# Kernel optimization log

Hardware: AMD Instinct MI355X
Metric: run time of the kernel (lower is better)

Reference implementation:

```python
import jax, jax.numpy as jnp
import numpy as np

jax.config.update("jax_enable_x64", True)  # loss accumulates int64 squared index diffs (~1e14)

PATCH, STRIDE = 7, 1


def extract_patches(img, p, s):
    # img: [b, c, h, w] -> patches [b, N, c*p*p], N = oh*ow (normalize_patch='none')
    pat = jax.lax.conv_general_dilated_patches(img, (p, p), (s, s), 'VALID')  # [b, c*p*p, oh, ow]
    b, d = pat.shape[0], pat.shape[1]
    return pat.reshape(b, d, -1).transpose(0, 2, 1)


def bisect_left(a, v):
    # Exact replica of np.searchsorted(a, v, side='left') binary search,
    # applied (as in the original code) to an UNSORTED int array `a`.
    # a: [N] int, v: [M] int -> [M] insertion indices in [0, N].
    N = a.shape[0]
    lo = jnp.zeros(v.shape, jnp.int64)
    hi = jnp.full(v.shape, N, jnp.int64)
    n_iter = int(np.ceil(np.log2(N))) + 1
    for _ in range(n_iter):
        mid = (lo + hi) // 2
        am = a[jnp.clip(mid, 0, N - 1)]
        go = lo < hi
        pred = am < v
        lo = jnp.where(go & pred, mid + 1, lo)
        hi = jnp.where(go & (~pred), mid, hi)
    return lo


def nearest_vals(a, v):
    # Vectorized find_nearest(a, v_i) for all v_i. a: [N], v: [M].
    N = a.shape[0]
    idx = bisect_left(a, v)
    a_prev = a[jnp.clip(idx - 1, 0, N - 1)]
    a_at = a[jnp.clip(idx, 0, N - 1)]
    take_prev = (idx > 0) & ((idx == N) | (jnp.abs(v - a_prev) < jnp.abs(v - a_at)))
    return jnp.where(take_prev, a_prev, a_at)


def reference(x, y, rand):
    # rand: [b, d, num_proj]; per-batch projection matrix, normalized by unbiased column std
    rand = rand / jnp.std(rand, axis=1, keepdims=True, ddof=1)
    xp = extract_patches(x, PATCH, STRIDE)  # [b, N, d]
    yp = extract_patches(y, PATCH, STRIDE)  # [b, N, d]
    proj_x = jnp.einsum('bnd,bdp->bnp', xp, rand)
    proj_y = jnp.einsum('bnd,bdp->bnp', yp, rand)
    # Original overwrites projections with argsort indices; only j=0 is used
    # because of the early return inside the projection loop.
    ai = jnp.argsort(proj_x[:, :, 0], axis=1).astype(jnp.int64)  # [b, N]
    at = jnp.argsort(proj_y[:, :, 0], axis=1).astype(jnp.int64)  # [b, N]
    nearest = jax.vmap(nearest_vals)(at, ai)  # [b, N]
    N = ai.shape[1]
    per_image = jnp.sum((ai - nearest) ** 2, axis=1) / N  # int sum -> float
    return jnp.mean(per_image)  # batch_reduction='mean'


def setup_inputs() -> dict:
    key = jax.random.key(0)
    k1, k2, k3 = jax.random.split(key, 3)
    b, c, h, w = 4, 3, 256, 256
    d = c * PATCH * PATCH  # 147
    x = jax.random.normal(k1, (b, c, h, w), dtype=jnp.float32)
    y = jax.random.normal(k2, (b, c, h, w), dtype=jnp.float32)
    rand = jax.random.normal(k3, (b, d, 1), dtype=jnp.float32)
    return {"x": x, "y": y, "rand": rand}
```

## Files before the change

kernel.cpp:

```cpp
#include <hip/hip_runtime.h>
#include <stdint.h>

#define OH 250
#define OW 250
#define NPTS (OH*OW)
#define NSEG 4
#define D 147
#define CH 3
#define IMH 256
#define IMW 256
#define NITER 17
#define NBUCK 8192
#define CAP 128
#define SIG0 12.124355652982141

typedef unsigned long long u64;
typedef unsigned int u32;

#define OFF_SREC  0UL
#define OFF_A     33554432UL
#define OFF_WTS   34554432UL
#define OFF_CURS  34559136UL
#define OFF_BASES 34690208UL
#define OFF_SUMS  34821296UL
#define OFF_TICK  34821328UL
#define OFF_OFLOW 34821336UL
#define WS_NEED   34821340UL

__device__ __forceinline__ u64 packd(double f) {
  u64 u = (u64)__double_as_longlong(f);
  return (u & 0x8000000000000000ULL) ? ~u : (u | 0x8000000000000000ULL);
}

__device__ __forceinline__ int bucket_of(u64 rec) {
  u64 t = rec & ~0x1FFFFULL;
  u64 bits = (t & 0x8000000000000000ULL) ? (t & 0x7FFFFFFFFFFFFFFFULL) : ~t;
  double v = __longlong_as_double((long long)bits);
  double z = (v + 4.0 * SIG0) * ((double)NBUCK / (8.0 * SIG0));
  int b = (z <= 0.0) ? 0 : (int)z;
  if (b > NBUCK - 1) b = NBUCK - 1;
  return b;
}

__global__ __launch_bounds__(256) void setup_kern(const float* __restrict__ rnd,
                                                  double* __restrict__ wts,
                                                  u32* __restrict__ curs,
                                                  u64* __restrict__ sums,
                                                  u32* __restrict__ tick,
                                                  u32* __restrict__ oflow) {
  int t = threadIdx.x;
  if (blockIdx.x < 4) {
    int b = blockIdx.x;
    int lane = t & 63;
    double v0 = (double)rnd[b * D + lane];
    double v1 = (double)rnd[b * D + lane + 64];
    double v2 = (lane + 128 < D) ? (double)rnd[b * D + lane + 128] : 0.0;
    double sm = v0 + v1 + v2;
    #pragma unroll
    for (int o = 32; o > 0; o >>= 1) sm += __shfl_xor(sm, o, 64);
    double mean = sm / (double)D;
    double d0 = v0 - mean, d1 = v1 - mean;
    double d2 = (lane + 128 < D) ? (v2 - mean) : 0.0;
    double ss = d0 * d0 + d1 * d1 + d2 * d2;
    #pragma unroll
    for (int o = 32; o > 0; o >>= 1) ss += __shfl_xor(ss, o, 64);
    double stdv = sqrt(ss / (double)(D - 1));
    if (t < 64) {
      wts[b * D + lane] = v0 / stdv;
      wts[b * D + lane + 64] = v1 / stdv;
      if (lane + 128 < D) wts[b * D + lane + 128] = v2 / stdv;
    }
    if (b == 0 && t < 8) ((u32*)sums)[t] = 0u;
    if (b == 0 && t >= 8 && t < 10) tick[t - 8] = 0u;
    if (b == 0 && t == 10) oflow[0] = 0u;
  } else {
    int g = (blockIdx.x - 4) * 1024 + t * 4;
    if (g < NSEG * NBUCK) {
      curs[g] = 0u; curs[g + 1] = 0u; curs[g + 2] = 0u; curs[g + 3] = 0u;
    }
  }
}

__global__ __launch_bounds__(256) void conv_kern(const float* __restrict__ y,
                                                 const double* __restrict__ wts,
                                                 u64* __restrict__ srec,
                                                 u32* __restrict__ curs,
                                                 u32* __restrict__ oflow) {
  __shared__ float tile[CH][22][22];
  __shared__ double wlds[D];
  int b = blockIdx.z;
  const float* in = y + (size_t)b * CH * IMH * IMW;
  int bi = blockIdx.y * 16, bj = blockIdx.x * 16;
  int tid = threadIdx.y * 16 + threadIdx.x;
  if (tid < D) wlds[tid] = wts[b * D + tid];
  for (int c = 0; c < CH; ++c)
    for (int t = tid; t < 22 * 22; t += 256) {
      int rr = t / 22, cc = t - rr * 22;
      int r = bi + rr, col = bj + cc;
      float v = 0.f;
      if (r < IMH && col < IMW) v = in[((size_t)c * IMH + r) * IMW + col];
      tile[c][rr][cc] = v;
    }
  __syncthreads();
  int i = bi + threadIdx.y, j = bj + threadIdx.x;
  if (i < OH && j < OW) {
    double acc = 0.0;
    #pragma unroll
    for (int c = 0; c < CH; ++c) {
      double ac = 0.0;
      #pragma unroll
      for (int ph = 0; ph < 7; ++ph)
        #pragma unroll
        for (int pw = 0; pw < 7; ++pw)
          ac = fma((double)tile[c][threadIdx.y + ph][threadIdx.x + pw],
                   wlds[c * 49 + ph * 7 + pw], ac);
      acc += ac;
    }
    int n = i * OW + j;
    u64 rec = (packd(acc) & ~0x1FFFFULL) | (u64)(u32)n;
    int bk = b * NBUCK + bucket_of(rec);
    u32 pos = atomicAdd(&curs[bk], 1u);
    if (pos < CAP) srec[(size_t)bk * CAP + pos] = rec;
    else atomicOr(oflow, 1u);
  }
}

__global__ __launch_bounds__(1024) void scan_kern(const u32* __restrict__ curs,
                                                  u32* __restrict__ bases,
                                                  u32* __restrict__ oflow) {
  __shared__ u32 part[1024];
  int seg = blockIdx.x, t = threadIdx.x;
  u32 c[8]; u32 run = 0;
  #pragma unroll
  for (int m = 0; m < 8; ++m) {
    u32 v = curs[seg * NBUCK + 8 * t + m];
    c[m] = v > CAP ? CAP : v;
    run += c[m];
  }
  part[t] = run;
  __syncthreads();
  for (int off = 1; off < 1024; off <<= 1) {
    u32 v = (t >= off) ? part[t - off] : 0u;
    __syncthreads();
    part[t] += v;
    __syncthreads();
  }
  u32 ex = part[t] - run;
  #pragma unroll
  for (int m = 0; m < 8; ++m) {
    bases[seg * (NBUCK + 1) + 8 * t + m] = ex;
    ex += c[m];
  }
  if (t == 1023) {
    bases[seg * (NBUCK + 1) + NBUCK] = ex;
    if (ex != NPTS) atomicOr(oflow, 2u);
  }
}

__global__ __launch_bounds__(512) void bsort_kern(const u64* __restrict__ srec,
                                                  const u32* __restrict__ bases,
                                                  u32* __restrict__ a) {
  __shared__ u64 buf[8][CAP];
  int wid = threadIdx.x >> 6, lane = threadIdx.x & 63;
  int B = blockIdx.x * 8 + wid;
  int seg = B / NBUCK, bk = B & (NBUCK - 1);
  u32 b0 = bases[seg * (NBUCK + 1) + bk];
  u32 b1 = bases[seg * (NBUCK + 1) + bk + 1];
  int n = (int)(b1 - b0);
  const u64* src = srec + (size_t)B * CAP;
  u32* dst = a + (size_t)seg * NPTS + b0;
  for (int i = lane; i < n; i += 64) buf[wid][i] = src[i];
  __syncthreads();
  for (int i = lane; i < n; i += 64) {
    u64 x = buf[wid][i];
    int r = 0;
    for (int j = 0; j < n; ++j) r += (buf[wid][j] < x);
    dst[r] = (u32)(x & 0x1FFFFULL);
  }
}

#define HALF (NSEG * NPTS / 2)
__global__ __launch_bounds__(256) void loss_kern(const u32* __restrict__ a_all,
                                                 u64* __restrict__ sums,
                                                 u32* __restrict__ tick,
                                                 const u32* __restrict__ oflow,
                                                 float* __restrict__ out,
                                                 int nblocks) {
  __shared__ u64 lsums[NSEG];
  __shared__ u32 rank_s;
  int tid = threadIdx.x;
  if (tid < NSEG) lsums[tid] = 0ULL;
  __syncthreads();
  int g = blockIdx.x * 256 + tid;
  if (g < HALF) {
    int g1 = g + HALF;
    int s0 = g / NPTS, s1 = g1 / NPTS;
    int vv0 = g - s0 * NPTS, vv1 = g1 - s1 * NPTS;
    const u32* A0 = a_all + (size_t)s0 * NPTS;
    const u32* A1 = a_all + (size_t)s1 * NPTS;
    int lo0 = 0, hi0 = NPTS, lo1 = 0, hi1 = NPTS;
    #pragma unroll
    for (int it = 0; it < NITER; ++it) {
      int mid0 = (lo0 + hi0) >> 1, mid1 = (lo1 + hi1) >> 1;
      int cm0 = mid0 > NPTS - 1 ? NPTS - 1 : mid0;
      int cm1 = mid1 > NPTS - 1 ? NPTS - 1 : mid1;
      int am0 = (int)A0[cm0];
      int am1 = (int)A1[cm1];
      if (lo0 < hi0) { if (am0 < vv0) lo0 = mid0 + 1; else hi0 = mid0; }
      if (lo1 < hi1) { if (am1 < vv1) lo1 = mid1 + 1; else hi1 = mid1; }
    }
    {
      int pi = lo0 - 1; if (pi < 0) pi = 0; if (pi > NPTS - 1) pi = NPTS - 1;
      int ci = lo0;     if (ci > NPTS - 1) ci = NPTS - 1;
      int ap = (int)A0[pi], aa = (int)A0[ci];
      int d1 = vv0 - ap; if (d1 < 0) d1 = -d1;
      int d2 = vv0 - aa; if (d2 < 0) d2 = -d2;
      bool tp = (lo0 > 0) && ((lo0 == NPTS) || (d1 < d2));
      long long dd = (long long)(vv0 - (tp ? ap : aa));
      atomicAdd(&lsums[s0], (u64)(dd * dd));
    }
    {
      int pi = lo1 - 1; if (pi < 0) pi = 0; if (pi > NPTS - 1) pi = NPTS - 1;
      int ci = lo1;     if (ci > NPTS - 1) ci = NPTS - 1;
      int ap = (int)A1[pi], aa = (int)A1[ci];
      int d1 = vv1 - ap; if (d1 < 0) d1 = -d1;
      int d2 = vv1 - aa; if (d2 < 0) d2 = -d2;
      bool tp = (lo1 > 0) && ((lo1 == NPTS) || (d1 < d2));
      long long dd = (long long)(vv1 - (tp ? ap : aa));
      atomicAdd(&lsums[s1], (u64)(dd * dd));
    }
  }
  __syncthreads();
  if (tid < NSEG && lsums[tid]) atomicAdd(&sums[tid], lsums[tid]);
  __syncthreads();
  if (tid == 0) {
    rank_s = atomicAdd(&tick[1], 1u);
    if (rank_s == (u32)(nblocks - 1)) {
      u32 of = __hip_atomic_load(oflow, __ATOMIC_RELAXED, __HIP_MEMORY_SCOPE_AGENT);
      if (of) { out[0] = 8.0e12f + 1.0e11f * (float)of; return; }
      double l = 0.0;
      for (int s = 0; s < NSEG; ++s) {
        u64 sv = __hip_atomic_load(&sums[s], __ATOMIC_RELAXED, __HIP_MEMORY_SCOPE_AGENT);
        l += (double)(long long)sv / (double)NPTS;
      }
      out[0] = (float)(l / 4.0);
    }
  }
}

__global__ void guard_kern(float* __restrict__ out) {
  if (threadIdx.x == 0 && blockIdx.x == 0) out[0] = 9.0e12f;
}

extern "C" void kernel_launch(void* const* d_in, const int* in_sizes, int n_in,
                              void* d_out, int out_size, void* d_ws, size_t ws_size,
                              hipStream_t stream) {
  (void)in_sizes; (void)n_in; (void)out_size;
  if (ws_size < WS_NEED) { guard_kern<<<1, 64, 0, stream>>>((float*)d_out); return; }
  const float* y   = (const float*)d_in[1];
  const float* rnd = (const float*)d_in[2];

  char* ws = (char*)d_ws;
  u64* srec   = (u64*)(ws + OFF_SREC);
  u32* aidx   = (u32*)(ws + OFF_A);
  double* wts = (double*)(ws + OFF_WTS);
  u32* curs   = (u32*)(ws + OFF_CURS);
  u32* bases  = (u32*)(ws + OFF_BASES);
  u64* sums   = (u64*)(ws + OFF_SUMS);
  u32* tick   = (u32*)(ws + OFF_TICK);
  u32* oflow  = (u32*)(ws + OFF_OFLOW);
  float* out  = (float*)d_out;

  setup_kern<<<36, 256, 0, stream>>>(rnd, wts, curs, sums, tick, oflow);
  conv_kern<<<dim3(16, 16, NSEG), dim3(16, 16), 0, stream>>>(y, wts, srec, curs, oflow);
  scan_kern<<<NSEG, 1024, 0, stream>>>(curs, bases, oflow);
  bsort_kern<<<NSEG * NBUCK / 8, 512, 0, stream>>>(srec, bases, aidx);
  int nb = (HALF + 255) / 256;
  loss_kern<<<nb, 256, 0, stream>>>(aidx, sums, tick, oflow, out, nb);
}
```

Measured before the change: 119.7 us.

## Fuse setup into conv and merge scan with bucket sort via flag handoff

The setup kernel is removed. Weight normalization is now computed redundantly per conv block directly into LDS, and zeroing becomes a single memset. The scan and bucket sort kernels are merged into one launch. The first four ticketed blocks compute per-segment prefix sums with a wave-shuffle scan and publish a release flag. All blocks compute local ranks first, then spin on the flag before scattering. This cuts two launches and a global round-trip, at the cost of a spin-wait that depends on forward progress and on tick being reused by the loss kernel.

```diff
diff --git a/kernel.cpp b/kernel.cpp
--- a/kernel.cpp
+++ b/kernel.cpp
@@ -19,13 +19,14 @@
 
 #define OFF_SREC  0UL
 #define OFF_A     33554432UL
-#define OFF_WTS   34554432UL
 #define OFF_CURS  34559136UL
 #define OFF_BASES 34690208UL
 #define OFF_SUMS  34821296UL
 #define OFF_TICK  34821328UL
 #define OFF_OFLOW 34821336UL
-#define WS_NEED   34821340UL
+#define OFF_FLAGS 34821340UL
+#define WS_NEED   34821356UL
+#define ZERO_BYTES (WS_NEED - OFF_CURS)
 
 __device__ __forceinline__ u64 packd(double f) {
   u64 u = (u64)__double_as_longlong(f);
@@ -42,57 +43,39 @@
   return b;
 }
 
-__global__ __launch_bounds__(256) void setup_kern(const float* __restrict__ rnd,
-                                                  double* __restrict__ wts,
-                                                  u32* __restrict__ curs,
-                                                  u64* __restrict__ sums,
-                                                  u32* __restrict__ tick,
-                                                  u32* __restrict__ oflow) {
-  int t = threadIdx.x;
-  if (blockIdx.x < 4) {
-    int b = blockIdx.x;
-    int lane = t & 63;
-    double v0 = (double)rnd[b * D + lane];
-    double v1 = (double)rnd[b * D + lane + 64];
-    double v2 = (lane + 128 < D) ? (double)rnd[b * D + lane + 128] : 0.0;
-    double sm = v0 + v1 + v2;
-    #pragma unroll
-    for (int o = 32; o > 0; o >>= 1) sm += __shfl_xor(sm, o, 64);
-    double mean = sm / (double)D;
-    double d0 = v0 - mean, d1 = v1 - mean;
-    double d2 = (lane + 128 < D) ? (v2 - mean) : 0.0;
-    double ss = d0 * d0 + d1 * d1 + d2 * d2;
-    #pragma unroll
-    for (int o = 32; o > 0; o >>= 1) ss += __shfl_xor(ss, o, 64);
-    double stdv = sqrt(ss / (double)(D - 1));
-    if (t < 64) {
-      wts[b * D + lane] = v0 / stdv;
-      wts[b * D + lane + 64] = v1 / stdv;
-      if (lane + 128 < D) wts[b * D + lane + 128] = v2 / stdv;
-    }
-    if (b == 0 && t < 8) ((u32*)sums)[t] = 0u;
-    if (b == 0 && t >= 8 && t < 10) tick[t - 8] = 0u;
-    if (b == 0 && t == 10) oflow[0] = 0u;
-  } else {
-    int g = (blockIdx.x - 4) * 1024 + t * 4;
-    if (g < NSEG * NBUCK) {
-      curs[g] = 0u; curs[g + 1] = 0u; curs[g + 2] = 0u; curs[g + 3] = 0u;
-    }
-  }
-}
-
 __global__ __launch_bounds__(256) void conv_kern(const float* __restrict__ y,
-                                                 const double* __restrict__ wts,
+                                                 const float* __restrict__ rnd,
                                                  u64* __restrict__ srec,
                                                  u32* __restrict__ curs,
                                                  u32* __restrict__ oflow) {
   __shared__ float tile[CH][22][22];
   __shared__ double wlds[D];
   int b = blockIdx.z;
+  int tid = threadIdx.y * 16 + threadIdx.x;
+  int lane = tid & 63;
+  {
+    const float* rb = rnd + b * D;
+    double v0 = (double)rb[lane];
+    double v1 = (double)rb[lane + 64];
+    double v2 = (lane + 128 < D) ? (double)rb[lane + 128] : 0.0;
+    double sm = v0 + v1 + v2;
+    #pragma unroll
+    for (int o = 32; o > 0; o >>= 1) sm += __shfl_xor(sm, o, 64);
+    double mean = sm / (double)D;
+    double d0 = v0 - mean, d1 = v1 - mean;
+    double d2 = (lane + 128 < D) ? (v2 - mean) : 0.0;
+    double ss = d0 * d0 + d1 * d1 + d2 * d2;
+    #pragma unroll
+    for (int o = 32; o > 0; o >>= 1) ss += __shfl_xor(ss, o, 64);
+    double stdv = sqrt(ss / (double)(D - 1));
+    if (tid < 64) {
+      wlds[lane] = v0 / stdv;
+      wlds[lane + 64] = v1 / stdv;
+      if (lane + 128 < D) wlds[lane + 128] = v2 / stdv;
+    }
+  }
   const float* in = y + (size_t)b * CH * IMH * IMW;
   int bi = blockIdx.y * 16, bj = blockIdx.x * 16;
-  int tid = threadIdx.y * 16 + threadIdx.x;
-  if (tid < D) wlds[tid] = wts[b * D + tid];
   for (int c = 0; c < CH; ++c)
     for (int t = tid; t < 22 * 22; t += 256) {
       int rr = t / 22, cc = t - rr * 22;
@@ -125,57 +108,93 @@
   }
 }
 
-__global__ __launch_bounds__(1024) void scan_kern(const u32* __restrict__ curs,
-                                                  u32* __restrict__ bases,
-                                                  u32* __restrict__ oflow) {
-  __shared__ u32 part[1024];
-  int seg = blockIdx.x, t = threadIdx.x;
-  u32 c[8]; u32 run = 0;
+__global__ __launch_bounds__(512) void bsortscan_kern(const u64* __restrict__ srec,
+                                                      const u32* __restrict__ curs,
+                                                      u32* __restrict__ bases,
+                                                      u32* __restrict__ flags,
+                                                      u32* __restrict__ tick,
+                                                      u32* __restrict__ a,
+                                                      u32* __restrict__ oflow) {
+  __shared__ u64 buf[8][CAP];
+  __shared__ u32 wsum[8];
+  __shared__ u32 ticket_s;
+  int tid = threadIdx.x;
+  int wid = tid >> 6, lane = tid & 63;
+  if (tid == 0) ticket_s = atomicAdd(&tick[0], 1u);
+  __syncthreads();
+  if (ticket_s < NSEG) {
+    int sseg = (int)ticket_s;
+    const u32* cs = curs + sseg * NBUCK;
+    u32 c[16]; u32 run = 0;
+    #pragma unroll
+    for (int m = 0; m < 16; ++m) {
+      u32 v = cs[tid * 16 + m];
+      c[m] = v > CAP ? CAP : v;
+      run += c[m];
+    }
+    u32 inc = run;
+    #pragma unroll
+    for (int o = 1; o < 64; o <<= 1) {
+      u32 v = __shfl_up(inc, o, 64);
+      if (lane >= o) inc += v;
+    }
+    if (lane == 63) wsum[wid] = inc;
+    __syncthreads();
+    u32 woff = 0;
+    for (int w2 = 0; w2 < wid; ++w2) woff += wsum[w2];
+    u32 ex = woff + inc - run;
+    u32* bs = bases + sseg * (NBUCK + 1);
+    #pragma unroll
+    for (int m = 0; m < 16; ++m) {
+      __hip_atomic_store(&bs[tid * 16 + m], ex, __ATOMIC_RELAXED, __HIP_MEMORY_SCOPE_AGENT);
+      ex += c[m];
+    }
+    if (tid == 511) {
+      __hip_atomic_store(&bs[NBUCK], ex, __ATOMIC_RELAXED, __HIP_MEMORY_SCOPE_AGENT);
+      if (ex != NPTS) atomicOr(oflow, 2u);
+    }
+    __syncthreads();
+    if (tid == 0)
+      __hip_atomic_store(&flags[sseg], 1u, __ATOMIC_RELEASE, __HIP_MEMORY_SCOPE_AGENT);
+  }
+  int blk = blockIdx.x;
+  int seg = blk >> 8;
+  int bk0 = (blk & 255) * 32 + wid * 4;
+  u64 x0[4], x1[4]; int rr0[4], rr1[4], nn[4];
   #pragma unroll
-  for (int m = 0; m < 8; ++m) {
-    u32 v = curs[seg * NBUCK + 8 * t + m];
-    c[m] = v > CAP ? CAP : v;
-    run += c[m];
-  }
-  part[t] = run;
-  __syncthreads();
-  for (int off = 1; off < 1024; off <<= 1) {
-    u32 v = (t >= off) ? part[t - off] : 0u;
-    __syncthreads();
-    part[t] += v;
-    __syncthreads();
-  }
-  u32 ex = part[t] - run;
+  for (int k = 0; k < 4; ++k) {
+    int B = seg * NBUCK + bk0 + k;
+    u32 v = curs[B];
+    int n = (int)(v > CAP ? CAP : v);
+    nn[k] = n;
+    const u64* src = srec + (size_t)B * CAP;
+    u64 a0 = (lane < n) ? src[lane] : ~0ULL;
+    u64 a1 = (lane + 64 < n) ? src[lane + 64] : ~0ULL;
+    if (lane < n) buf[wid][lane] = a0;
+    if (lane + 64 < n) buf[wid][lane + 64] = a1;
+    int r0 = 0, r1 = 0;
+    for (int j = 0; j < n; ++j) {
+      u64 bj = buf[wid][j];
+      r0 += (bj < a0);
+      r1 += (bj < a1);
+    }
+    x0[k] = a0; x1[k] = a1; rr0[k] = r0; rr1[k] = r1;
+  }
+  if (tid == 0) {
+    while (__hip_atomic_load(&flags[seg], __ATOMIC_RELAXED, __HIP_MEMORY_SCOPE_AGENT) == 0u)
+      __builtin_amdgcn_s_sleep(16);
+  }
+  __syncthreads();
+  (void)__hip_atomic_load(&flags[seg], __ATOMIC_ACQUIRE, __HIP_MEMORY_SCOPE_AGENT);
+  const u32* bs = bases + seg * (NBUCK + 1);
+  u32* aseg = a + (size_t)seg * NPTS;
   #pragma unroll
-  for (int m = 0; m < 8; ++m) {
-    bases[seg * (NBUCK + 1) + 8 * t + m] = ex;
-    ex += c[m];
-  }
-  if (t == 1023) {
-    bases[seg * (NBUCK + 1) + NBUCK] = ex;
-    if (ex != NPTS) atomicOr(oflow, 2u);
-  }
-}
-
-__global__ __launch_bounds__(512) void bsort_kern(const u64* __restrict__ srec,
-                                                  const u32* __restrict__ bases,
-                                                  u32* __restrict__ a) {
-  __shared__ u64 buf[8][CAP];
-  int wid = threadIdx.x >> 6, lane = threadIdx.x & 63;
-  int B = blockIdx.x * 8 + wid;
-  int seg = B / NBUCK, bk = B & (NBUCK - 1);
-  u32 b0 = bases[seg * (NBUCK + 1) + bk];
-  u32 b1 = bases[seg * (NBUCK + 1) + bk + 1];
-  int n = (int)(b1 - b0);
-  const u64* src = srec + (size_t)B * CAP;
-  u32* dst = a + (size_t)seg * NPTS + b0;
-  for (int i = lane; i < n; i += 64) buf[wid][i] = src[i];
-  __syncthreads();
-  for (int i = lane; i < n; i += 64) {
-    u64 x = buf[wid][i];
-    int r = 0;
-    for (int j = 0; j < n; ++j) r += (buf[wid][j] < x);
-    dst[r] = (u32)(x & 0x1FFFFULL);
+  for (int k = 0; k < 4; ++k) {
+    int n = nn[k];
+    u32 b0 = __hip_atomic_load(&bs[bk0 + k], __ATOMIC_RELAXED, __HIP_MEMORY_SCOPE_AGENT);
+    u32* dst = aseg + b0;
+    if (lane < n) dst[rr0[k]] = (u32)(x0[k] & 0x1FFFFULL);
+    if (lane + 64 < n) dst[rr1[k]] = (u32)(x1[k] & 0x1FFFFULL);
   }
 }
 
@@ -263,18 +282,17 @@
   char* ws = (char*)d_ws;
   u64* srec   = (u64*)(ws + OFF_SREC);
   u32* aidx   = (u32*)(ws + OFF_A);
-  double* wts = (double*)(ws + OFF_WTS);
   u32* curs   = (u32*)(ws + OFF_CURS);
   u32* bases  = (u32*)(ws + OFF_BASES);
   u64* sums   = (u64*)(ws + OFF_SUMS);
   u32* tick   = (u32*)(ws + OFF_TICK);
   u32* oflow  = (u32*)(ws + OFF_OFLOW);
+  u32* flags  = (u32*)(ws + OFF_FLAGS);
   float* out  = (float*)d_out;
 
-  setup_kern<<<36, 256, 0, stream>>>(rnd, wts, curs, sums, tick, oflow);
-  conv_kern<<<dim3(16, 16, NSEG), dim3(16, 16), 0, stream>>>(y, wts, srec, curs, oflow);
-  scan_kern<<<NSEG, 1024, 0, stream>>>(curs, bases, oflow);
-  bsort_kern<<<NSEG * NBUCK / 8, 512, 0, stream>>>(srec, bases, aidx);
+  hipMemsetAsync(ws + OFF_CURS, 0, ZERO_BYTES, stream);
+  conv_kern<<<dim3(16, 16, NSEG), dim3(16, 16), 0, stream>>>(y, rnd, srec, curs, oflow);
+  bsortscan_kern<<<1024, 512, 0, stream>>>(srec, curs, bases, flags, tick, aidx, oflow);
   int nb = (HALF + 255) / 256;
   loss_kern<<<nb, 256, 0, stream>>>(aidx, sums, tick, oflow, out, nb);
 }
```

After: 191.9 us. 1.6x slower.

## Fuse weight normalization into conv, register-block 4 outputs per thread, memset workspace

Applied to the files above, without the earlier changes.

Removes the separate setup kernel: each conv block recomputes the std-normalized projection weights directly into LDS, and the counters are zeroed with hipMemsetAsync. The conv now uses 32x32 output tiles where each thread computes four horizontally adjacent outputs with a sliding register window, reusing tile loads across outputs. The aim is fewer launches and fewer LDS reads per FMA, at the cost of redundant weight normalization in every block and fewer, larger blocks (256 instead of 1024).

```diff
diff --git a/kernel.cpp b/kernel.cpp
--- a/kernel.cpp
+++ b/kernel.cpp
@@ -13,19 +13,20 @@
 #define NBUCK 8192
 #define CAP 128
 #define SIG0 12.124355652982141
+#define TSTR 49
 
 typedef unsigned long long u64;
 typedef unsigned int u32;
 
 #define OFF_SREC  0UL
 #define OFF_A     33554432UL
-#define OFF_WTS   34554432UL
 #define OFF_CURS  34559136UL
 #define OFF_BASES 34690208UL
 #define OFF_SUMS  34821296UL
 #define OFF_TICK  34821328UL
 #define OFF_OFLOW 34821336UL
 #define WS_NEED   34821340UL
+#define ZERO_BYTES (WS_NEED - OFF_CURS)
 
 __device__ __forceinline__ u64 packd(double f) {
   u64 u = (u64)__double_as_longlong(f);
@@ -42,19 +43,21 @@
   return b;
 }
 
-__global__ __launch_bounds__(256) void setup_kern(const float* __restrict__ rnd,
-                                                  double* __restrict__ wts,
-                                                  u32* __restrict__ curs,
-                                                  u64* __restrict__ sums,
-                                                  u32* __restrict__ tick,
-                                                  u32* __restrict__ oflow) {
-  int t = threadIdx.x;
-  if (blockIdx.x < 4) {
-    int b = blockIdx.x;
-    int lane = t & 63;
-    double v0 = (double)rnd[b * D + lane];
-    double v1 = (double)rnd[b * D + lane + 64];
-    double v2 = (lane + 128 < D) ? (double)rnd[b * D + lane + 128] : 0.0;
+__global__ __launch_bounds__(256) void conv_kern(const float* __restrict__ y,
+                                                 const float* __restrict__ rnd,
+                                                 u64* __restrict__ srec,
+                                                 u32* __restrict__ curs,
+                                                 u32* __restrict__ oflow) {
+  __shared__ float tile[CH][38][TSTR];
+  __shared__ double wlds[D];
+  int b = blockIdx.z;
+  int tid = threadIdx.x;
+  int lane = tid & 63;
+  {
+    const float* rb = rnd + b * D;
+    double v0 = (double)rb[lane];
+    double v1 = (double)rb[lane + 64];
+    double v2 = (lane + 128 < D) ? (double)rb[lane + 128] : 0.0;
     double sm = v0 + v1 + v2;
     #pragma unroll
     for (int o = 32; o > 0; o >>= 1) sm += __shfl_xor(sm, o, 64);
@@ -65,63 +68,63 @@
     #pragma unroll
     for (int o = 32; o > 0; o >>= 1) ss += __shfl_xor(ss, o, 64);
     double stdv = sqrt(ss / (double)(D - 1));
-    if (t < 64) {
-      wts[b * D + lane] = v0 / stdv;
-      wts[b * D + lane + 64] = v1 / stdv;
-      if (lane + 128 < D) wts[b * D + lane + 128] = v2 / stdv;
-    }
-    if (b == 0 && t < 8) ((u32*)sums)[t] = 0u;
-    if (b == 0 && t >= 8 && t < 10) tick[t - 8] = 0u;
-    if (b == 0 && t == 10) oflow[0] = 0u;
-  } else {
-    int g = (blockIdx.x - 4) * 1024 + t * 4;
-    if (g < NSEG * NBUCK) {
-      curs[g] = 0u; curs[g + 1] = 0u; curs[g + 2] = 0u; curs[g + 3] = 0u;
-    }
-  }
-}
-
-__global__ __launch_bounds__(256) void conv_kern(const float* __restrict__ y,
-                                                 const double* __restrict__ wts,
-                                                 u64* __restrict__ srec,
-                                                 u32* __restrict__ curs,
-                                                 u32* __restrict__ oflow) {
-  __shared__ float tile[CH][22][22];
-  __shared__ double wlds[D];
-  int b = blockIdx.z;
+    if (tid < 64) {
+      wlds[lane] = v0 / stdv;
+      wlds[lane + 64] = v1 / stdv;
+      if (lane + 128 < D) wlds[lane + 128] = v2 / stdv;
+    }
+  }
   const float* in = y + (size_t)b * CH * IMH * IMW;
-  int bi = blockIdx.y * 16, bj = blockIdx.x * 16;
-  int tid = threadIdx.y * 16 + threadIdx.x;
-  if (tid < D) wlds[tid] = wts[b * D + tid];
+  int bi = blockIdx.y * 32, bj = blockIdx.x * 32;
   for (int c = 0; c < CH; ++c)
-    for (int t = tid; t < 22 * 22; t += 256) {
-      int rr = t / 22, cc = t - rr * 22;
+    for (int t = tid; t < 38 * 38; t += 256) {
+      int rr = t / 38, cc = t - rr * 38;
       int r = bi + rr, col = bj + cc;
       float v = 0.f;
       if (r < IMH && col < IMW) v = in[((size_t)c * IMH + r) * IMW + col];
       tile[c][rr][cc] = v;
     }
   __syncthreads();
-  int i = bi + threadIdx.y, j = bj + threadIdx.x;
-  if (i < OH && j < OW) {
-    double acc = 0.0;
-    #pragma unroll
-    for (int c = 0; c < CH; ++c) {
-      double ac = 0.0;
+  int oy = tid >> 3;
+  int ox = (tid & 7) << 2;
+  int i = bi + oy;
+  double acc0 = 0.0, acc1 = 0.0, acc2 = 0.0, acc3 = 0.0;
+  #pragma unroll
+  for (int c = 0; c < CH; ++c) {
+    double a0 = 0.0, a1 = 0.0, a2 = 0.0, a3 = 0.0;
+    #pragma unroll
+    for (int ph = 0; ph < 7; ++ph) {
+      const float* trow = &tile[c][oy + ph][ox];
+      double w0 = (double)trow[0];
+      double w1 = (double)trow[1];
+      double w2 = (double)trow[2];
       #pragma unroll
-      for (int ph = 0; ph < 7; ++ph)
-        #pragma unroll
-        for (int pw = 0; pw < 7; ++pw)
-          ac = fma((double)tile[c][threadIdx.y + ph][threadIdx.x + pw],
-                   wlds[c * 49 + ph * 7 + pw], ac);
-      acc += ac;
-    }
-    int n = i * OW + j;
-    u64 rec = (packd(acc) & ~0x1FFFFULL) | (u64)(u32)n;
-    int bk = b * NBUCK + bucket_of(rec);
-    u32 pos = atomicAdd(&curs[bk], 1u);
-    if (pos < CAP) srec[(size_t)bk * CAP + pos] = rec;
-    else atomicOr(oflow, 1u);
+      for (int pw = 0; pw < 7; ++pw) {
+        double w3 = (double)trow[pw + 3];
+        double wt = wlds[c * 49 + ph * 7 + pw];
+        a0 = fma(w0, wt, a0);
+        a1 = fma(w1, wt, a1);
+        a2 = fma(w2, wt, a2);
+        a3 = fma(w3, wt, a3);
+        w0 = w1; w1 = w2; w2 = w3;
+      }
+    }
+    acc0 += a0; acc1 += a1; acc2 += a2; acc3 += a3;
+  }
+  if (i < OH) {
+    double av[4] = {acc0, acc1, acc2, acc3};
+    #pragma unroll
+    for (int jj = 0; jj < 4; ++jj) {
+      int j = bj + ox + jj;
+      if (j < OW) {
+        int n = i * OW + j;
+        u64 rec = (packd(av[jj]) & ~0x1FFFFULL) | (u64)(u32)n;
+        int bk = b * NBUCK + bucket_of(rec);
+        u32 pos = atomicAdd(&curs[bk], 1u);
+        if (pos < CAP) srec[(size_t)bk * CAP + pos] = rec;
+        else atomicOr(oflow, 1u);
+      }
+    }
   }
 }
 
@@ -263,7 +266,6 @@
   char* ws = (char*)d_ws;
   u64* srec   = (u64*)(ws + OFF_SREC);
   u32* aidx   = (u32*)(ws + OFF_A);
-  double* wts = (double*)(ws + OFF_WTS);
   u32* curs   = (u32*)(ws + OFF_CURS);
   u32* bases  = (u32*)(ws + OFF_BASES);
   u64* sums   = (u64*)(ws + OFF_SUMS);
@@ -271,8 +273,8 @@
   u32* oflow  = (u32*)(ws + OFF_OFLOW);
   float* out  = (float*)d_out;
 
-  setup_kern<<<36, 256, 0, stream>>>(rnd, wts, curs, sums, tick, oflow);
-  conv_kern<<<dim3(16, 16, NSEG), dim3(16, 16), 0, stream>>>(y, wts, srec, curs, oflow);
+  hipMemsetAsync(ws + OFF_CURS, 0, ZERO_BYTES, stream);
+  conv_kern<<<dim3(8, 8, NSEG), 256, 0, stream>>>(y, rnd, srec, curs, oflow);
   scan_kern<<<NSEG, 1024, 0, stream>>>(curs, bases, oflow);
   bsort_kern<<<NSEG * NBUCK / 8, 512, 0, stream>>>(srec, bases, aidx);
   int nb = (HALF + 255) / 256;
```

Result: slower. 207.3 us (+73.2%).
